# Kernel optimization log

Measured on AMD Instinct MI355X. Metric: run time of the kernel, lower is better.

Reference implementation:

```python
import jax, jax.numpy as jnp
import numpy as np

NEG = -1e20  # finite stand-in for -inf (exp underflows to 0; avoids nan grads)
S_RANGE = 19   # prune_range hard-coded in the module
TERM = 0       # termination/blank symbol
LM_ONLY = 0.25 # lm_only_scale; am_only_scale = 0 so that branch vanishes


def _mi(px, py):
    """RNN-T mutual-information forward DP (fast_rnnt mutual_information_recursion).
    px: (B,S,T+1) logprob of emitting symbol s+1 at (s,t); py: (B,S+1,T) blank logprobs.
    p[b,s,t] = logaddexp(p[b,s-1,t]+px[b,s-1,t], p[b,s,t-1]+py[b,s,t-1]); returns p[:,S,T]."""
    B, S, T1 = px.shape
    p0 = jnp.concatenate([jnp.zeros((B, 1), px.dtype),
                          jnp.cumsum(py[:, 0, :], axis=1)], axis=1)  # row s=0: (B,T+1)
    def outer(p_prev, inp):
        px_s, py_s = inp                 # (B,T+1), (B,T)
        b = p_prev + px_s                # vertical (emit) path into next row
        def inner(c, xs):
            b_t, py_t = xs
            c = jnp.logaddexp(b_t, c + py_t)
            return c, c
        _, rest = jax.lax.scan(inner, b[:, 0], (b[:, 1:].T, py_s.T))  # rest: (T,B)
        p_row = jnp.concatenate([b[:, :1], rest.T], axis=1)
        return p_row, None
    p_last, _ = jax.lax.scan(outer, p0,
                             (jnp.moveaxis(px, 1, 0), jnp.moveaxis(py[:, 1:, :], 1, 0)))
    return p_last[:, -1]  # (B,) total log-prob at (S,T)


def _smoothed_logprobs(am, lm, symbols):
    """fast_rnnt.get_rnnt_logprobs_smoothed with lm_only_scale=0.25, am_only_scale=0."""
    B, T, C = am.shape
    S = symbols.shape[1]
    lm_max = jnp.max(lm, axis=2, keepdims=True)   # (B,S+1,1)
    am_max = jnp.max(am, axis=2, keepdims=True)   # (B,T,1)
    lm_p = jnp.exp(lm - lm_max)
    am_p = jnp.exp(am - am_max)
    # normalizers[b,s,t] = log sum_k exp(lm[b,s,k] + am[b,t,k]) via matmul trick
    normalizers = jnp.log(jnp.einsum('bsc,btc->bst', lm_p, am_p)) \
        + lm_max + jnp.swapaxes(am_max, 1, 2)     # (B,S+1,T)
    sym_b = jnp.broadcast_to(symbols[:, None, :], (B, T, S))
    px_am = jnp.swapaxes(jnp.take_along_axis(am, sym_b, axis=2), 1, 2)  # (B,S,T)
    px_lm = jnp.take_along_axis(lm[:, :S], symbols[:, :, None], axis=2)  # (B,S,1)
    px = px_am + px_lm - normalizers[:, :S, :]
    lm_lsm = jax.nn.log_softmax(lm, axis=2)
    px_lmonly = jnp.take_along_axis(lm_lsm[:, :S], symbols[:, :, None], axis=2)
    comb = 1.0 - LM_ONLY
    px_i = comb * px + LM_ONLY * px_lmonly
    px_i = jnp.concatenate([px_i, jnp.full((B, S, 1), NEG, px_i.dtype)], axis=2)  # (B,S,T+1)
    py = am[:, :, TERM][:, None, :] + lm[:, :, TERM][:, :, None] - normalizers
    py_i = comb * py + LM_ONLY * lm_lsm[:, :, TERM][:, :, None]  # (B,S+1,T)
    return px_i, py_i


def _suffix_min(x):  # fast_rnnt _monotonic_lower_bound: x[t] = min(x[t:])
    return jax.lax.associative_scan(jnp.minimum, x, axis=1, reverse=True)


def _adjust_lower_bound(s_begin, r):  # fast_rnnt _adjust_pruning_lower_bound
    Tn = s_begin.shape[1]
    s_begin = _suffix_min(s_begin)
    off = (r - 1) * jnp.arange(Tn, dtype=s_begin.dtype)
    y = -(s_begin - off)
    y = jnp.maximum(_suffix_min(y), 0)
    return -(y - off)


def _prune_ranges(px_grad, py_grad, r):
    """fast_rnnt.get_rnnt_prune_ranges (all sequences full length)."""
    B, S, T1 = px_grad.shape
    T = T1 - 1
    py_pad = jnp.concatenate([py_grad, jnp.zeros((B, S + 1, 1), py_grad.dtype)], axis=2)
    tot = jnp.concatenate([px_grad, jnp.zeros((B, 1, T1), px_grad.dtype)], axis=1) + py_pad
    tot = jnp.concatenate([jnp.zeros((B, 1, T1), tot.dtype), tot], axis=1)  # (B,S+2,T1)
    cs = jnp.cumsum(tot, axis=1)
    diff = cs[:, r:, :] - cs[:, :-r, :]  # windowed occupancy sums
    s_begin = jnp.argmax(diff, axis=1)[:, :T].astype(jnp.int32)
    s_begin = _adjust_lower_bound(s_begin, r)
    return s_begin[:, :, None] + jnp.arange(r, dtype=jnp.int32)[None, None, :]  # (B,T,r)


def _pruned_logprobs(logits, symbols, ranges):
    """fast_rnnt.get_rnnt_logprobs_pruned."""
    B, T, r, C = logits.shape
    S = symbols.shape[1]
    norm = jax.nn.logsumexp(logits, axis=3)  # (B,T,r)
    sym_t = jnp.concatenate([symbols, jnp.full((B, 1), TERM, symbols.dtype)], axis=1)
    sym_b = jnp.broadcast_to(sym_t[:, None, :], (B, T, S + 1))
    pruned_sym = jnp.take_along_axis(sym_b, ranges, axis=2)  # (B,T,r)
    px = jnp.take_along_axis(logits, pruned_sym[..., None], axis=3)[..., 0] - norm
    py = logits[..., TERM] - norm
    def to_full(x):  # scatter (B,T,r) band into absolute symbol positions (B,T,S+1)
        pad = jnp.full((B, T, S + 1 - r), NEG, x.dtype)
        xf = jnp.concatenate([x, pad], axis=2)
        idx = (jnp.arange(S + 1)[None, None, :] - ranges[:, :, 0:1]) % (S + 1)
        return jnp.take_along_axis(xf, idx, axis=2)
    px_f = jnp.swapaxes(to_full(px), 1, 2)  # (B,S+1,T)
    py_f = jnp.swapaxes(to_full(py), 1, 2)  # (B,S+1,T)
    px_f = jnp.concatenate([px_f, jnp.full((B, S + 1, 1), NEG, px_f.dtype)], axis=2)[:, :S, :]
    return px_f, py_f  # (B,S,T+1), (B,S+1,T)


def _forward(am, lm, targets, joiner_w, joiner_b):
    px, py = _smoothed_logprobs(am, lm, targets)
    simple_loss = -jnp.mean(_mi(px, py))  # reduction='mean'
    # occupation-probability grads (values only, used for pruning)
    gpx, gpy = jax.grad(lambda a: jnp.sum(_mi(a[0], a[1])))(
        (jax.lax.stop_gradient(px), jax.lax.stop_gradient(py)))
    ranges = _prune_ranges(gpx, gpy, S_RANGE)  # (B,T,19) int32, constant wrt grads
    lm_pruned = jax.vmap(lambda l, rg: l[rg])(lm, ranges)  # (B,T,r,C) gather
    # joiner: logits = Linear(tanh(am_pruned + lm_pruned)); am broadcast over r
    logits = jnp.einsum('btrc,cd->btrd',
                        jnp.tanh(am[:, :, None, :] + lm_pruned), joiner_w) + joiner_b
    px2, py2 = _pruned_logprobs(logits.astype(jnp.float32), targets, ranges)
    pruned_loss = -jnp.mean(_mi(px2, py2))
    return 0.1 * simple_loss + pruned_loss


def setup_inputs() -> dict:
    key = jax.random.key(0)
    k = jax.random.split(key, 5)
    B, T, S, C = 8, 512, 128, 512
    return {
        "am": jax.random.normal(k[0], (B, T, C), jnp.float32),
        "lm": jax.random.normal(k[1], (B, S + 1, C), jnp.float32),
        "targets": jax.random.randint(k[2], (B, S), 1, C),  # blank=0 excluded
        "y_lens": jnp.full((B,), S, jnp.int32),             # full-length boundaries
        "joiner_w": 0.05 * jax.random.normal(k[3], (C, C), jnp.float32),
        "joiner_b": jnp.zeros((C,), jnp.float32),
    }


def reference(am, lm, targets, y_lens, joiner_w, joiner_b):
    # boundary = [0, 0, y_lens(=S), T] for every sequence
    return _forward(am, lm, targets, joiner_w, joiner_b)
```

## Files before the change

### kernel.cpp

```cpp
#include <hip/hip_runtime.h>
#include <math.h>

#define NEGV -1e20f
#define DPAD 132
#define RBOFF 16
#define ROWSA 676
#define RB(p,b) ((p) + ((size_t)(b) * ROWSA + RBOFF) * DPAD)

typedef __attribute__((ext_vector_type(4))) float floatx4;
typedef __attribute__((ext_vector_type(8))) short short8;
typedef __attribute__((ext_vector_type(4))) short short4v;


__device__ __forceinline__ float lae(float a, float b){
  float mx = fmaxf(a, b);
  float mn = fminf(a, b);
  return mx + __logf(1.f + __expf(mn - mx));
}

__device__ __forceinline__ short f2bf(float x){
  union { float f; unsigned u; } v; v.f = x;
  unsigned r = v.u + 0x7fffu + ((v.u >> 16) & 1u);
  return (short)(r >> 16);
}

__device__ __forceinline__ float fast_tanh(float x){
  x = fminf(fmaxf(x, -15.f), 15.f);
  float e = __expf(2.f * x);
  return (e - 1.f) / (e + 1.f);
}

__global__ __launch_bounds__(256) void k_row_stats(
    const float* __restrict__ in, float* __restrict__ outMax, float* __restrict__ outLse)
{
  int row = blockIdx.x;
  const float* r = in + (size_t)row * 512;
  int tid = threadIdx.x;
  float v0 = r[tid], v1 = r[tid + 256];
  float m = fmaxf(v0, v1);
  #pragma unroll
  for (int off = 32; off; off >>= 1) m = fmaxf(m, __shfl_xor(m, off, 64));
  __shared__ float sm[4];
  __shared__ float sbm;
  int wv = tid >> 6;
  if ((tid & 63) == 0) sm[wv] = m;
  __syncthreads();
  if (tid == 0) sbm = fmaxf(fmaxf(sm[0], sm[1]), fmaxf(sm[2], sm[3]));
  __syncthreads();
  float mx = sbm;
  if (tid == 0) outMax[row] = mx;
  if (outLse){
    float s = __expf(v0 - mx) + __expf(v1 - mx);
    #pragma unroll
    for (int off = 32; off; off >>= 1) s += __shfl_xor(s, off, 64);
    __shared__ float sp[4];
    if ((tid & 63) == 0) sp[wv] = s;
    __syncthreads();
    if (tid == 0) outLse[row] = mx + __logf(sp[0] + sp[1] + sp[2] + sp[3]);
  }
}

__global__ __launch_bounds__(256) void k_wb(const float* __restrict__ W, short* __restrict__ Wb){
  int idx = blockIdx.x * 256 + threadIdx.x;
  int d = idx >> 9, c = idx & 511;
  Wb[idx] = f2bf(W[c * 512 + d]);
}

__global__ __launch_bounds__(256) void k_norm(
    const float* __restrict__ am, const float* __restrict__ lm,
    const float* __restrict__ lmMax, const float* __restrict__ amMax,
    float* __restrict__ normv)
{
  int b = blockIdx.z;
  int s0 = blockIdx.y * 16;
  int t0 = blockIdx.x * 128;
  __shared__ float lmS[16][68];
  __shared__ float amS[128][68];
  int tid = threadIdx.x;
  int ts = tid >> 4, tt = tid & 15;
  float acc[8];
  #pragma unroll
  for (int j = 0; j < 8; ++j) acc[j] = 0.f;

  for (int k0 = 0; k0 < 512; k0 += 64){
    {
      int e = tid * 4;
      int rr = e >> 6, cc = e & 63;
      int s = s0 + rr;
      floatx4 o = {0.f, 0.f, 0.f, 0.f};
      if (s < 129){
        float mx = lmMax[b * 129 + s];
        floatx4 v = *(const floatx4*)(lm + ((size_t)(b * 129 + s)) * 512 + k0 + cc);
        o[0] = __expf(v[0] - mx); o[1] = __expf(v[1] - mx);
        o[2] = __expf(v[2] - mx); o[3] = __expf(v[3] - mx);
      }
      *(floatx4*)&lmS[rr][cc] = o;
    }
    #pragma unroll
    for (int i = 0; i < 8; ++i){
      int e = (tid + i * 256) * 4;
      int rr = e >> 6, cc = e & 63;
      float mx = amMax[b * 512 + t0 + rr];
      floatx4 v = *(const floatx4*)(am + ((size_t)(b * 512 + t0 + rr)) * 512 + k0 + cc);
      floatx4 o;
      o[0] = __expf(v[0] - mx); o[1] = __expf(v[1] - mx);
      o[2] = __expf(v[2] - mx); o[3] = __expf(v[3] - mx);
      *(floatx4*)&amS[rr][cc] = o;
    }
    __syncthreads();
    #pragma unroll 4
    for (int k = 0; k < 64; ++k){
      float a = lmS[ts][k];
      #pragma unroll
      for (int j = 0; j < 8; ++j) acc[j] += a * amS[tt + 16 * j][k];
    }
    __syncthreads();
  }
  int s = s0 + ts;
  if (s < 129){
    float lmx = lmMax[b * 129 + s];
    #pragma unroll
    for (int j = 0; j < 8; ++j){
      int t = t0 + tt + 16 * j;
      normv[((size_t)(b * 129 + s)) * 512 + t] = __logf(acc[j]) + lmx + amMax[b * 512 + t];
    }
  }
}

__global__ __launch_bounds__(256) void k_pxpy(
    const float* __restrict__ am, const float* __restrict__ lm,
    const int* __restrict__ targets, const float* __restrict__ normv,
    const float* __restrict__ lmLse, float* __restrict__ pxd, float* __restrict__ pyd)
{
  int bs = blockIdx.x;
  int b = bs / 129, s = bs % 129;
  float lm0 = lm[(size_t)bs * 512];
  float lse = lmLse[bs];
  int sym = 0; float lms = 0.f;
  if (s < 128){ sym = targets[b * 128 + s]; lms = lm[(size_t)bs * 512 + sym]; }
  const float* nrm = normv + (size_t)bs * 512;
  float* pydb = RB(pyd, b);
  float* pxdb = RB(pxd, b);
  for (int t = threadIdx.x; t < 513; t += 256){
    if (t < 512){
      float n = nrm[t];
      float a0 = am[((size_t)(b * 512 + t)) * 512];
      pydb[(size_t)(s + t) * DPAD + s] = 0.75f * (a0 + lm0 - n) + 0.25f * (lm0 - lse);
      if (s < 128){
        float as = am[((size_t)(b * 512 + t)) * 512 + sym];
        pxdb[(size_t)(s + t) * DPAD + s] = 0.75f * (as + lms - n) + 0.25f * (lms - lse);
      }
    } else if (s < 128){
      pxdb[(size_t)(s + 512) * DPAD + s] = NEGV;
    }
  }
}


__device__ __forceinline__ void dp_fwd_run(
    const float* __restrict__ pxb, const float* __restrict__ pyb,
    float* __restrict__ pab, float* __restrict__ tot, int b)
{
  int l = threadIdx.x;
  const int a = 2 * l;
  float curA = NEGV, curB = NEGV, curC = NEGV, send = NEGV;
  int paddr = (l - 1) << 2;

  float2 cpx = *(const float2*)(pxb - DPAD + a);
  float2 cpy = *(const float2*)(pyb - DPAD + a);
  float  cpz = pyb[-DPAD + 128];

  float2 b0px[8], b0py[8], b1px[8], b1py[8];
  float  b0pz[8], b1pz[8];
  float  outx[8], outy[8], outc[8];

  #pragma unroll
  for (int j = 0; j < 8; ++j){
    b0px[j] = *(const float2*)(pxb + (size_t)j * DPAD + a);
    b0py[j] = *(const float2*)(pyb + (size_t)j * DPAD + a);
    b0pz[j] = pyb[(size_t)j * DPAD + 128];
  }

  for (int i = 0; i < 40; ++i){
    int d0 = i * 16;
    #pragma unroll
    for (int j = 0; j < 8; ++j){
      b1px[j] = *(const float2*)(pxb + (size_t)(d0 + 8 + j) * DPAD + a);
      b1py[j] = *(const float2*)(pyb + (size_t)(d0 + 8 + j) * DPAD + a);
      b1pz[j] = pyb[(size_t)(d0 + 8 + j) * DPAD + 128];
    }
    #pragma unroll
    for (int j = 0; j < 8; ++j){
      int d = d0 + j;
      float2 pxm = j ? b0px[j - 1] : cpx;
      float2 pym = j ? b0py[j - 1] : cpy;
      float  pzm = j ? b0pz[j - 1] : cpz;
      float recv = __int_as_float(
          __builtin_amdgcn_ds_bpermute(paddr, __float_as_int(send)));
      int tA = d - a, tC = d - 128;
      float aaA = (l > 0) ? recv : NEGV;
      float bbA = (tA >= 1) ? curA + pym.x : NEGV;
      float nvA = lae(aaA, bbA);
      if (l == 0 && d == 0) nvA = 0.f;
      float aaB = curA + pxm.x;
      float bbB = (tA >= 2) ? curB + pym.y : NEGV;
      float nvB = lae(aaB, bbB);
      float aaC = curB + pxm.y;
      float bbC = (tC >= 1) ? curC + pzm : NEGV;
      float nvC = lae(aaC, bbC);
      if (tA >= 0 && tA <= 512) curA = nvA;
      if (tA >= 1 && tA <= 513) curB = nvB;
      if (tC >= 0 && tC <= 512) curC = nvC;
      send = curB + b0px[j].y;
      outx[j] = curA; outy[j] = curB; outc[j] = curC;
    }
    cpx = b0px[7]; cpy = b0py[7]; cpz = b0pz[7];
    if (pab){
      #pragma unroll
      for (int j = 0; j < 8; ++j)
        *(float2*)(pab + (size_t)(d0 + j) * DPAD + a) = make_float2(outx[j], outy[j]);
      if (l == 63){
        #pragma unroll
        for (int j = 0; j < 8; ++j)
          pab[(size_t)(d0 + j) * DPAD + 128] = outc[j];
      }
    }
    #pragma unroll
    for (int j = 0; j < 8; ++j){
      b0px[j] = *(const float2*)(pxb + (size_t)(d0 + 16 + j) * DPAD + a);
      b0py[j] = *(const float2*)(pyb + (size_t)(d0 + 16 + j) * DPAD + a);
      b0pz[j] = pyb[(size_t)(d0 + 16 + j) * DPAD + 128];
    }
    #pragma unroll
    for (int j = 0; j < 8; ++j){
      int d = d0 + 8 + j;
      float2 pxm = j ? b1px[j - 1] : cpx;
      float2 pym = j ? b1py[j - 1] : cpy;
      float  pzm = j ? b1pz[j - 1] : cpz;
      float recv = __int_as_float(
          __builtin_amdgcn_ds_bpermute(paddr, __float_as_int(send)));
      int tA = d - a, tC = d - 128;
      float aaA = (l > 0) ? recv : NEGV;
      float bbA = (tA >= 1) ? curA + pym.x : NEGV;
      float nvA = lae(aaA, bbA);
      float aaB = curA + pxm.x;
      float bbB = (tA >= 2) ? curB + pym.y : NEGV;
      float nvB = lae(aaB, bbB);
      float aaC = curB + pxm.y;
      float bbC = (tC >= 1) ? curC + pzm : NEGV;
      float nvC = lae(aaC, bbC);
      if (tA >= 0 && tA <= 512) curA = nvA;
      if (tA >= 1 && tA <= 513) curB = nvB;
      if (tC >= 0 && tC <= 512) curC = nvC;
      send = curB + b1px[j].y;
      outx[j] = curA; outy[j] = curB; outc[j] = curC;
    }
    cpx = b1px[7]; cpy = b1py[7]; cpz = b1pz[7];
    if (pab){
      #pragma unroll
      for (int j = 0; j < 8; ++j)
        *(float2*)(pab + (size_t)(d0 + 8 + j) * DPAD + a) = make_float2(outx[j], outy[j]);
      if (l == 63){
        #pragma unroll
        for (int j = 0; j < 8; ++j)
          pab[(size_t)(d0 + 8 + j) * DPAD + 128] = outc[j];
      }
    }
  }
  {
    float aaC = curB + cpx.y;
    float bbC = curC + cpz;
    curC = lae(aaC, bbC);
    if (l == 63){
      if (pab) pab[(size_t)640 * DPAD + 128] = curC;
      tot[b] = curC;
    }
  }
}

__device__ __forceinline__ void dp_bwd_run(
    const float* __restrict__ pxb, const float* __restrict__ pyb,
    float* __restrict__ beb)
{
  int l = threadIdx.x;
  const int a = 2 * l;
  float curA = NEGV, curB = NEGV, curC = NEGV, send = NEGV;
  int paddr = (l + 1) << 2;

  float2 b0px[8], b0py[8], b1px[8], b1py[8];
  float  b0pz[8], b1pz[8];
  float  outx[8], outy[8], outc[8];

  #pragma unroll
  for (int j = 0; j < 8; ++j){
    b0px[j] = *(const float2*)(pxb + (size_t)(640 - j) * DPAD + a);
    b0py[j] = *(const float2*)(pyb + (size_t)(640 - j) * DPAD + a);
    b0pz[j] = pyb[(size_t)(640 - j) * DPAD + 128];
  }

  for (int i = 0; i < 40; ++i){
    int d0 = 640 - 16 * i;
    #pragma unroll
    for (int j = 0; j < 8; ++j){
      b1px[j] = *(const float2*)(pxb + (size_t)(d0 - 8 - j) * DPAD + a);
      b1py[j] = *(const float2*)(pyb + (size_t)(d0 - 8 - j) * DPAD + a);
      b1pz[j] = pyb[(size_t)(d0 - 8 - j) * DPAD + 128];
    }
    #pragma unroll
    for (int j = 0; j < 8; ++j){
      int d = d0 - j;
      float2 pxA = b0px[j]; float2 pyA = b0py[j]; float pzA = b0pz[j];
      float recv = __int_as_float(
          __builtin_amdgcn_ds_bpermute(paddr, __float_as_int(send)));
      int tA = d - a, tB = tA - 1, tC = d - 128;
      float aaA = pxA.x + curB;
      float bbA = (tA <= 511) ? pyA.x + curA : NEGV;
      float nvA = lae(aaA, bbA);
      float up = (l < 63) ? recv : curC;
      float aaB = pxA.y + up;
      float bbB = (tB <= 511) ? pyA.y + curB : NEGV;
      float nvB = lae(aaB, bbB);
      float nvC = (tC <= 511) ? pzA + curC : NEGV;
      if (tC == 512) nvC = 0.f;
      if (tA >= 0 && tA <= 512) curA = nvA;
      if (tB >= 0 && tB <= 512) curB = nvB;
      if (tC >= 0 && tC <= 512) curC = nvC;
      send = curA;
      outx[j] = curA; outy[j] = curB; outc[j] = curC;
    }
    #pragma unroll
    for (int j = 0; j < 8; ++j)
      *(float2*)(beb + (size_t)(d0 - j) * DPAD + a) = make_float2(outx[j], outy[j]);
    if (l == 63){
      #pragma unroll
      for (int j = 0; j < 8; ++j)
        beb[(size_t)(d0 - j) * DPAD + 128] = outc[j];
    }
    #pragma unroll
    for (int j = 0; j < 8; ++j){
      b0px[j] = *(const float2*)(pxb + (size_t)(d0 - 16 - j) * DPAD + a);
      b0py[j] = *(const float2*)(pyb + (size_t)(d0 - 16 - j) * DPAD + a);
      b0pz[j] = pyb[(size_t)(d0 - 16 - j) * DPAD + 128];
    }
    #pragma unroll
    for (int j = 0; j < 8; ++j){
      int d = d0 - 8 - j;
      float2 pxA = b1px[j]; float2 pyA = b1py[j]; float pzA = b1pz[j];
      float recv = __int_as_float(
          __builtin_amdgcn_ds_bpermute(paddr, __float_as_int(send)));
      int tA = d - a, tB = tA - 1, tC = d - 128;
      float aaA = pxA.x + curB;
      float bbA = (tA <= 511) ? pyA.x + curA : NEGV;
      float nvA = lae(aaA, bbA);
      float up = (l < 63) ? recv : curC;
      float aaB = pxA.y + up;
      float bbB = (tB <= 511) ? pyA.y + curB : NEGV;
      float nvB = lae(aaB, bbB);
      float nvC = (tC <= 511) ? pzA + curC : NEGV;
      if (tC == 512) nvC = 0.f;
      if (tA >= 0 && tA <= 512) curA = nvA;
      if (tB >= 0 && tB <= 512) curB = nvB;
      if (tC >= 0 && tC <= 512) curC = nvC;
      send = curA;
      outx[j] = curA; outy[j] = curB; outc[j] = curC;
    }
    #pragma unroll
    for (int j = 0; j < 8; ++j)
      *(float2*)(beb + (size_t)(d0 - 8 - j) * DPAD + a) = make_float2(outx[j], outy[j]);
    if (l == 63){
      #pragma unroll
      for (int j = 0; j < 8; ++j)
        beb[(size_t)(d0 - 8 - j) * DPAD + 128] = outc[j];
    }
  }
  {
    float2 pxA = b0px[0]; float2 pyA = b0py[0]; float pzA = b0pz[0];
    float recv = __int_as_float(
        __builtin_amdgcn_ds_bpermute(paddr, __float_as_int(send)));
    int tA = -a, tB = tA - 1, tC = -128;
    float aaA = pxA.x + curB;
    float bbA = (tA <= 511) ? pyA.x + curA : NEGV;
    float nvA = lae(aaA, bbA);
    float up = (l < 63) ? recv : curC;
    float aaB = pxA.y + up;
    float bbB = (tB <= 511) ? pyA.y + curB : NEGV;
    float nvB = lae(aaB, bbB);
    (void)tC;
    if (tA >= 0 && tA <= 512) curA = nvA;
    if (tB >= 0 && tB <= 512) curB = nvB;
    *(float2*)(beb + a) = make_float2(curA, curB);
    if (l == 63) beb[128] = curC;
  }
}

__global__ __launch_bounds__(64) void k_dp_fb(
    const float* __restrict__ pxd, const float* __restrict__ pyd,
    float* __restrict__ pad, float* __restrict__ betad, float* __restrict__ tots)
{
  int blk = blockIdx.x;
  if (blk < 8){
    int b = blk;
    dp_fwd_run(RB(pxd, b), RB(pyd, b), RB(pad, b), tots, b);
  } else {
    int b = blk - 8;
    dp_bwd_run(RB(pxd, b), RB(pyd, b), RB(betad, b));
  }
}

__global__ __launch_bounds__(64) void k_dp_f2(
    const float* __restrict__ pxd, const float* __restrict__ pyd,
    float* __restrict__ totp)
{
  int b = blockIdx.x;
  dp_fwd_run(RB(pxd, b), RB(pyd, b), (float*)nullptr, totp, b);
}

__global__ __launch_bounds__(256) void k_window(
    const float* __restrict__ pxd, const float* __restrict__ pyd,
    const float* __restrict__ pad, const float* __restrict__ betad,
    const float* __restrict__ tots, int* __restrict__ sbr)
{
  __shared__ float tote[129][66];
  int b = blockIdx.x >> 3;
  int t0 = (blockIdx.x & 7) << 6;
  const float* px = RB(pxd, b);
  const float* py = RB(pyd, b);
  const float* pa = RB(pad, b);
  const float* be = RB(betad, b);
  float tv = tots[b];
  int tid = threadIdx.x;
  int wv = tid >> 6, ln = tid & 63;
  for (int dd = wv; dd < 192; dd += 4){
    int d = t0 + dd;
    int slo = dd - 63 > 0 ? dd - 63 : 0;
    int shi = dd < 128 ? dd : 128;
    int s = slo + ln;
    if (s <= shi){
      size_t r0 = (size_t)d * DPAD + s, r1 = (size_t)(d + 1) * DPAD + s;
      float pav = pa[r0];
      float v = __expf(pav + py[r0] + be[r1] - tv);
      if (s < 128) v += __expf(pav + px[r0] + be[r1 + 1] - tv);
      tote[s][dd - s] = v;
    }
  }
  __syncthreads();
  if (tid < 64){
    int c = tid;
    float win = 0.f;
    for (int s = 0; s < 19; ++s) win += tote[s][c];
    float best = win; int arg = 0;
    for (int w2 = 1; w2 <= 110; ++w2){
      win += tote[w2 + 18][c] - tote[w2 - 1][c];
      if (win > best){ best = win; arg = w2; }
    }
    sbr[b * 512 + t0 + c] = arg;
  }
}

__global__ void k_adjust(const int* __restrict__ sbr, int* __restrict__ sbeg){
  if (threadIdx.x != 0) return;
  int b = blockIdx.x;
  const int* in = sbr + b * 512;
  int* out = sbeg + b * 512;
  int sbm = 1 << 30, ym = 1 << 30;
  for (int t = 511; t >= 0; --t){
    sbm = min(sbm, in[t]);
    int y = 18 * t - sbm;
    ym = min(ym, y);
    int yc = ym > 0 ? ym : 0;
    out[t] = 18 * t - yc;
  }
}

__global__ __launch_bounds__(256) void k_joiner(
    const float* __restrict__ am, const float* __restrict__ lm,
    const int* __restrict__ targets, const float* __restrict__ bias,
    const short* __restrict__ Wb, const int* __restrict__ sbeg,
    float* __restrict__ pxv, float* __restrict__ pyv)
{
  __shared__ short Hs[32][40];
  __shared__ int rowSym[32];
  __shared__ int rowAm[32];
  __shared__ int rowLm[32];
  __shared__ float redM[32][4];
  __shared__ float redS[32][4];
  __shared__ float rowMax[32];
  __shared__ float rowNorm[32];

  int tid = threadIdx.x;
  int r0 = blockIdx.x * 32;
  if (tid < 32){
    int row = r0 + tid;
    int g = row / 19;
    int j = row - g * 19;
    int b = g >> 9;
    int t = g & 511;
    int start = sbeg[b * 512 + t];
    int sidx = start + j;
    rowSym[tid] = (sidx < 128) ? targets[b * 128 + sidx] : 0;
    rowAm[tid] = (b * 512 + t) * 512;
    rowLm[tid] = (b * 129 + sidx) * 512;
  }
  __syncthreads();

  int wv = tid >> 6, lane = tid & 63, q = lane >> 4, ln = lane & 15;
  int colBase = wv * 128 + ln;
  int hr = tid >> 3, kk = (tid & 7) * 4;

  floatx4 acc[2][8];
  #pragma unroll
  for (int mt = 0; mt < 2; ++mt)
    #pragma unroll
    for (int nt = 0; nt < 8; ++nt) acc[mt][nt] = (floatx4){0.f, 0.f, 0.f, 0.f};

  for (int k0 = 0; k0 < 512; k0 += 32){
    {
      const float* ap = am + (size_t)rowAm[hr] + k0 + kk;
      const float* lp = lm + (size_t)rowLm[hr] + k0 + kk;
      floatx4 a4 = *(const floatx4*)ap;
      floatx4 l4 = *(const floatx4*)lp;
      short4v h;
      h[0] = f2bf(fast_tanh(a4[0] + l4[0]));
      h[1] = f2bf(fast_tanh(a4[1] + l4[1]));
      h[2] = f2bf(fast_tanh(a4[2] + l4[2]));
      h[3] = f2bf(fast_tanh(a4[3] + l4[3]));
      *(short4v*)&Hs[hr][kk] = h;
    }
    __syncthreads();
    short8 afr0 = *(const short8*)&Hs[ln][q * 8];
    short8 afr1 = *(const short8*)&Hs[16 + ln][q * 8];
    #pragma unroll
    for (int nt = 0; nt < 8; ++nt){
      int col = colBase + nt * 16;
      short8 bfr = *(const short8*)(Wb + (size_t)col * 512 + k0 + q * 8);
      acc[0][nt] = __builtin_amdgcn_mfma_f32_16x16x32_bf16(afr0, bfr, acc[0][nt], 0, 0, 0);
      acc[1][nt] = __builtin_amdgcn_mfma_f32_16x16x32_bf16(afr1, bfr, acc[1][nt], 0, 0, 0);
    }
    __syncthreads();
  }

  #pragma unroll
  for (int nt = 0; nt < 8; ++nt){
    float bc = bias[colBase + nt * 16];
    #pragma unroll
    for (int mt = 0; mt < 2; ++mt)
      #pragma unroll
      for (int r = 0; r < 4; ++r) acc[mt][nt][r] += bc;
  }
  #pragma unroll
  for (int mt = 0; mt < 2; ++mt)
    #pragma unroll
    for (int r = 0; r < 4; ++r){
      int row = mt * 16 + q * 4 + r;
      float m = acc[mt][0][r];
      #pragma unroll
      for (int nt = 1; nt < 8; ++nt) m = fmaxf(m, acc[mt][nt][r]);
      m = fmaxf(m, __shfl_xor(m, 1, 16));
      m = fmaxf(m, __shfl_xor(m, 2, 16));
      m = fmaxf(m, __shfl_xor(m, 4, 16));
      m = fmaxf(m, __shfl_xor(m, 8, 16));
      if (ln == 0) redM[row][wv] = m;
    }
  __syncthreads();
  if (tid < 32) rowMax[tid] = fmaxf(fmaxf(redM[tid][0], redM[tid][1]),
                                    fmaxf(redM[tid][2], redM[tid][3]));
  __syncthreads();
  #pragma unroll
  for (int mt = 0; mt < 2; ++mt)
    #pragma unroll
    for (int r = 0; r < 4; ++r){
      int row = mt * 16 + q * 4 + r;
      float rm = rowMax[row];
      float sa = 0.f;
      #pragma unroll
      for (int nt = 0; nt < 8; ++nt) sa += __expf(acc[mt][nt][r] - rm);
      sa += __shfl_xor(sa, 1, 16);
      sa += __shfl_xor(sa, 2, 16);
      sa += __shfl_xor(sa, 4, 16);
      sa += __shfl_xor(sa, 8, 16);
      if (ln == 0) redS[row][wv] = sa;
    }
  __syncthreads();
  if (tid < 32) rowNorm[tid] = rowMax[tid] +
      __logf(redS[tid][0] + redS[tid][1] + redS[tid][2] + redS[tid][3]);
  __syncthreads();
  #pragma unroll
  for (int mt = 0; mt < 2; ++mt)
    #pragma unroll
    for (int nt = 0; nt < 8; ++nt){
      int col = colBase + nt * 16;
      #pragma unroll
      for (int r = 0; r < 4; ++r){
        int row = mt * 16 + q * 4 + r;
        float v = acc[mt][nt][r] - rowNorm[row];
        int gr = r0 + row;
        if (col == 0) pyv[gr] = v;
        if (col == rowSym[row]) pxv[gr] = v;
      }
    }
}

__global__ __launch_bounds__(192) void k_band(
    const float* __restrict__ pxv, const float* __restrict__ pyv,
    const int* __restrict__ sbeg, float* __restrict__ px2d, float* __restrict__ py2d)
{
  int bd = blockIdx.x;
  int b = bd / 640, d = bd - b * 640;
  int s = threadIdx.x;
  int t = d - s;
  if (s > 128 || t < 0 || t > 512) return;
  size_t addr = ((size_t)b * ROWSA + RBOFF + d) * DPAD + s;
  if (s < 128){
    float v;
    if (t == 512) v = NEGV;
    else {
      int start = sbeg[b * 512 + t];
      int j = s - start;
      v = (j >= 0 && j < 19) ? pxv[((size_t)(b * 512 + t)) * 19 + j] : NEGV;
    }
    px2d[addr] = v;
  }
  if (t <= 511){
    int start = sbeg[b * 512 + t];
    int j = s - start;
    py2d[addr] = (j >= 0 && j < 19) ? pyv[((size_t)(b * 512 + t)) * 19 + j] : NEGV;
  }
}

__global__ void k_final(const float* __restrict__ tots, const float* __restrict__ totp,
                        float* __restrict__ out){
  if (blockIdx.x == 0 && threadIdx.x == 0){
    float a = 0.f, c = 0.f;
    for (int i = 0; i < 8; ++i){ a += tots[i]; c += totp[i]; }
    out[0] = -0.1f * (a * 0.125f) - (c * 0.125f);
  }
}

extern "C" void kernel_launch(void* const* d_in, const int* in_sizes, int n_in,
                              void* d_out, int out_size, void* d_ws, size_t ws_size,
                              hipStream_t stream){
  (void)in_sizes; (void)n_in; (void)out_size; (void)ws_size;
  const float* am      = (const float*)d_in[0];
  const float* lm      = (const float*)d_in[1];
  const int*   targets = (const int*)d_in[2];
  const float* W       = (const float*)d_in[4];
  const float* bias    = (const float*)d_in[5];
  float* out = (float*)d_out;

  char* base = (char*)d_ws;
  size_t off = 0;
  auto alloc = [&](size_t bytes) -> char* {
    char* r = base + off;
    off += (bytes + 255) & ~(size_t)255;
    return r;
  };
  const size_t DARR = 8ull * ROWSA * DPAD * 4;
  float* amMax = (float*)alloc(8ull * 512 * 4);
  float* lmMax = (float*)alloc(8ull * 129 * 4);
  float* lmLse = (float*)alloc(8ull * 129 * 4);
  float* normv = (float*)alloc(8ull * 129 * 512 * 4);
  float* pxd   = (float*)alloc(DARR);
  float* pyd   = (float*)alloc(DARR);
  float* pad   = (float*)alloc(DARR);
  float* betad = (float*)alloc(DARR);
  float* tots  = (float*)alloc(8 * 4);
  float* totp  = (float*)alloc(8 * 4);
  int*   sbr   = (int*)alloc(8ull * 512 * 4);
  int*   sbeg  = (int*)alloc(8ull * 512 * 4);
  float* pxv   = (float*)alloc(8ull * 512 * 19 * 4);
  float* pyv   = (float*)alloc(8ull * 512 * 19 * 4);
  short* Wb    = (short*)alloc(512ull * 512 * 2);
  float* px2d  = pxd;
  float* py2d  = pyd;

  k_row_stats<<<dim3(4096), dim3(256), 0, stream>>>(am, amMax, (float*)nullptr);
  k_row_stats<<<dim3(1032), dim3(256), 0, stream>>>(lm, lmMax, lmLse);
  k_wb<<<dim3(1024), dim3(256), 0, stream>>>(W, Wb);
  k_norm<<<dim3(4, 9, 8), dim3(256), 0, stream>>>(am, lm, lmMax, amMax, normv);
  k_pxpy<<<dim3(1032), dim3(256), 0, stream>>>(am, lm, targets, normv, lmLse, pxd, pyd);
  k_dp_fb<<<dim3(16), dim3(64), 0, stream>>>(pxd, pyd, pad, betad, tots);
  k_window<<<dim3(64), dim3(256), 0, stream>>>(pxd, pyd, pad, betad, tots, sbr);
  k_adjust<<<dim3(8), dim3(64), 0, stream>>>(sbr, sbeg);
  k_joiner<<<dim3(2432), dim3(256), 0, stream>>>(am, lm, targets, bias, Wb, sbeg, pxv, pyv);
  k_band<<<dim3(5120), dim3(192), 0, stream>>>(pxv, pyv, sbeg, px2d, py2d);
  k_dp_f2<<<dim3(8), dim3(64), 0, stream>>>(px2d, py2d, totp);
  k_final<<<dim3(1), dim3(64), 0, stream>>>(tots, totp, out);
}
```

Before: 642.7 us.

## Enlarge joiner row tile and stage full tanh hidden row in LDS

The joiner kernel now processes 64 rows per block instead of 32. It precomputes the full 512-wide bf16 tanh(am+lm) tile into LDS once, so the K loop no longer needs per-step loads and barriers. Each W fragment load is now reused across four MFMA row tiles, which halves global traffic on the weight matrix. The cost is about 66KB of LDS plus more accumulator registers, which lowers occupancy and halves the grid to 1216 blocks.

```diff
diff --git a/kernel.cpp b/kernel.cpp
--- a/kernel.cpp
+++ b/kernel.cpp
@@ -377,7 +377,7 @@
     float2 pxA = b0px[0]; float2 pyA = b0py[0]; float pzA = b0pz[0];
     float recv = __int_as_float(
         __builtin_amdgcn_ds_bpermute(paddr, __float_as_int(send)));
-    int tA = -a, tB = tA - 1, tC = -128;
+    int tA = -a, tB = tA - 1;
     float aaA = pxA.x + curB;
     float bbA = (tA <= 511) ? pyA.x + curA : NEGV;
     float nvA = lae(aaA, bbA);
@@ -385,7 +385,7 @@
     float aaB = pxA.y + up;
     float bbB = (tB <= 511) ? pyA.y + curB : NEGV;
     float nvB = lae(aaB, bbB);
-    (void)tC;
+    (void)pzA;
     if (tA >= 0 && tA <= 512) curA = nvA;
     if (tB >= 0 && tB <= 512) curB = nvB;
     *(float2*)(beb + a) = make_float2(curA, curB);
@@ -472,24 +472,27 @@
   }
 }
 
+#define JROWS 64
+#define HSTR  520
+
 __global__ __launch_bounds__(256) void k_joiner(
     const float* __restrict__ am, const float* __restrict__ lm,
     const int* __restrict__ targets, const float* __restrict__ bias,
     const short* __restrict__ Wb, const int* __restrict__ sbeg,
     float* __restrict__ pxv, float* __restrict__ pyv)
 {
-  __shared__ short Hs[32][40];
-  __shared__ int rowSym[32];
-  __shared__ int rowAm[32];
-  __shared__ int rowLm[32];
-  __shared__ float redM[32][4];
-  __shared__ float redS[32][4];
-  __shared__ float rowMax[32];
-  __shared__ float rowNorm[32];
+  __shared__ short Hs[JROWS][HSTR];
+  __shared__ int rowSym[JROWS];
+  __shared__ int rowAm[JROWS];
+  __shared__ int rowLm[JROWS];
+  __shared__ float redM[JROWS][4];
+  __shared__ float redS[JROWS][4];
+  __shared__ float rowMax[JROWS];
+  __shared__ float rowNorm[JROWS];
 
   int tid = threadIdx.x;
-  int r0 = blockIdx.x * 32;
-  if (tid < 32){
+  int r0 = blockIdx.x * JROWS;
+  if (tid < JROWS){
     int row = r0 + tid;
     int g = row / 19;
     int j = row - g * 19;
@@ -503,52 +506,67 @@
   }
   __syncthreads();
 
+  {
+    int row = tid >> 2;
+    int kb = (tid & 3) * 8;
+    const float* ap = am + (size_t)rowAm[row];
+    const float* lp = lm + (size_t)rowLm[row];
+    #pragma unroll 4
+    for (int i = 0; i < 16; ++i){
+      int k = kb + i * 32;
+      floatx4 a0 = *(const floatx4*)(ap + k);
+      floatx4 a1 = *(const floatx4*)(ap + k + 4);
+      floatx4 l0 = *(const floatx4*)(lp + k);
+      floatx4 l1 = *(const floatx4*)(lp + k + 4);
+      short8 h;
+      h[0] = f2bf(fast_tanh(a0[0] + l0[0]));
+      h[1] = f2bf(fast_tanh(a0[1] + l0[1]));
+      h[2] = f2bf(fast_tanh(a0[2] + l0[2]));
+      h[3] = f2bf(fast_tanh(a0[3] + l0[3]));
+      h[4] = f2bf(fast_tanh(a1[0] + l1[0]));
+      h[5] = f2bf(fast_tanh(a1[1] + l1[1]));
+      h[6] = f2bf(fast_tanh(a1[2] + l1[2]));
+      h[7] = f2bf(fast_tanh(a1[3] + l1[3]));
+      *(short8*)&Hs[row][k] = h;
+    }
+  }
+  __syncthreads();
+
   int wv = tid >> 6, lane = tid & 63, q = lane >> 4, ln = lane & 15;
   int colBase = wv * 128 + ln;
-  int hr = tid >> 3, kk = (tid & 7) * 4;
-
-  floatx4 acc[2][8];
-  #pragma unroll
-  for (int mt = 0; mt < 2; ++mt)
+
+  floatx4 acc[4][8];
+  #pragma unroll
+  for (int mt = 0; mt < 4; ++mt)
     #pragma unroll
     for (int nt = 0; nt < 8; ++nt) acc[mt][nt] = (floatx4){0.f, 0.f, 0.f, 0.f};
 
+  #pragma unroll 2
   for (int k0 = 0; k0 < 512; k0 += 32){
-    {
-      const float* ap = am + (size_t)rowAm[hr] + k0 + kk;
-      const float* lp = lm + (size_t)rowLm[hr] + k0 + kk;
-      floatx4 a4 = *(const floatx4*)ap;
-      floatx4 l4 = *(const floatx4*)lp;
-      short4v h;
-      h[0] = f2bf(fast_tanh(a4[0] + l4[0]));
-      h[1] = f2bf(fast_tanh(a4[1] + l4[1]));
-      h[2] = f2bf(fast_tanh(a4[2] + l4[2]));
-      h[3] = f2bf(fast_tanh(a4[3] + l4[3]));
-      *(short4v*)&Hs[hr][kk] = h;
-    }
-    __syncthreads();
-    short8 afr0 = *(const short8*)&Hs[ln][q * 8];
-    short8 afr1 = *(const short8*)&Hs[16 + ln][q * 8];
+    short8 af[4];
+    #pragma unroll
+    for (int mt = 0; mt < 4; ++mt)
+      af[mt] = *(const short8*)&Hs[mt * 16 + ln][k0 + q * 8];
     #pragma unroll
     for (int nt = 0; nt < 8; ++nt){
       int col = colBase + nt * 16;
       short8 bfr = *(const short8*)(Wb + (size_t)col * 512 + k0 + q * 8);
-      acc[0][nt] = __builtin_amdgcn_mfma_f32_16x16x32_bf16(afr0, bfr, acc[0][nt], 0, 0, 0);
-      acc[1][nt] = __builtin_amdgcn_mfma_f32_16x16x32_bf16(afr1, bfr, acc[1][nt], 0, 0, 0);
-    }
-    __syncthreads();
+      #pragma unroll
+      for (int mt = 0; mt < 4; ++mt)
+        acc[mt][nt] = __builtin_amdgcn_mfma_f32_16x16x32_bf16(af[mt], bfr, acc[mt][nt], 0, 0, 0);
+    }
   }
 
   #pragma unroll
   for (int nt = 0; nt < 8; ++nt){
     float bc = bias[colBase + nt * 16];
     #pragma unroll
-    for (int mt = 0; mt < 2; ++mt)
+    for (int mt = 0; mt < 4; ++mt)
       #pragma unroll
       for (int r = 0; r < 4; ++r) acc[mt][nt][r] += bc;
   }
   #pragma unroll
-  for (int mt = 0; mt < 2; ++mt)
+  for (int mt = 0; mt < 4; ++mt)
     #pragma unroll
     for (int r = 0; r < 4; ++r){
       int row = mt * 16 + q * 4 + r;
@@ -562,11 +580,11 @@
       if (ln == 0) redM[row][wv] = m;
     }
   __syncthreads();
-  if (tid < 32) rowMax[tid] = fmaxf(fmaxf(redM[tid][0], redM[tid][1]),
-                                    fmaxf(redM[tid][2], redM[tid][3]));
-  __syncthreads();
-  #pragma unroll
-  for (int mt = 0; mt < 2; ++mt)
+  if (tid < JROWS) rowMax[tid] = fmaxf(fmaxf(redM[tid][0], redM[tid][1]),
+                                       fmaxf(redM[tid][2], redM[tid][3]));
+  __syncthreads();
+  #pragma unroll
+  for (int mt = 0; mt < 4; ++mt)
     #pragma unroll
     for (int r = 0; r < 4; ++r){
       int row = mt * 16 + q * 4 + r;
@@ -581,11 +599,11 @@
       if (ln == 0) redS[row][wv] = sa;
     }
   __syncthreads();
-  if (tid < 32) rowNorm[tid] = rowMax[tid] +
+  if (tid < JROWS) rowNorm[tid] = rowMax[tid] +
       __logf(redS[tid][0] + redS[tid][1] + redS[tid][2] + redS[tid][3]);
   __syncthreads();
   #pragma unroll
-  for (int mt = 0; mt < 2; ++mt)
+  for (int mt = 0; mt < 4; ++mt)
     #pragma unroll
     for (int nt = 0; nt < 8; ++nt){
       int col = colBase + nt * 16;
@@ -681,7 +699,7 @@
   k_dp_fb<<<dim3(16), dim3(64), 0, stream>>>(pxd, pyd, pad, betad, tots);
   k_window<<<dim3(64), dim3(256), 0, stream>>>(pxd, pyd, pad, betad, tots, sbr);
   k_adjust<<<dim3(8), dim3(64), 0, stream>>>(sbr, sbeg);
-  k_joiner<<<dim3(2432), dim3(256), 0, stream>>>(am, lm, targets, bias, Wb, sbeg, pxv, pyv);
+  k_joiner<<<dim3(1216), dim3(256), 0, stream>>>(am, lm, targets, bias, Wb, sbeg, pxv, pyv);
   k_band<<<dim3(5120), dim3(192), 0, stream>>>(pxv, pyv, sbeg, px2d, py2d);
   k_dp_f2<<<dim3(8), dim3(64), 0, stream>>>(px2d, py2d, totp);
   k_final<<<dim3(1), dim3(64), 0, stream>>>(tots, totp, out);
```

Result: no change. 632.9 us (-1.5%).
